# Optimization experiments

Measured on AMD Instinct MI355X. Metric: run time of the kernel, lower is better.

## Reference

```python
import jax, jax.numpy as jnp
import numpy as np

BS, H, W = 2, 24, 24
WIDTH = 20
M1 = M2 = 12
N = H * W
NPAIR = N * (N - 1) // 2
COLL_COEF = 0.9  # training=True path (eval path zeroes the collision term entirely)
_IU, _JU = np.triu_indices(N, k=1)  # static pair indices


def _gelu(x):
    return jax.nn.gelu(x, approximate=False)  # torch F.gelu default = exact erf


def _spectral(x, wr, wi):
    # x: (bs, c, h, w); wr/wi: (2, c, c, M1, M2) -> weights1, weights2
    bs, c, h, w = x.shape
    xft = jnp.fft.rfft2(x)  # (bs, c, h, w//2+1) complex64
    w1 = wr[0] + 1j * wi[0]
    w2 = wr[1] + 1j * wi[1]
    top = jnp.einsum('bixy,ioxy->boxy', xft[:, :, :M1, :M2], w1)
    bot = jnp.einsum('bixy,ioxy->boxy', xft[:, :, -M1:, :M2], w2)
    out = jnp.zeros((bs, c, h, w // 2 + 1), dtype=xft.dtype)
    out = out.at[:, :, :M1, :M2].set(top).at[:, :, -M1:, :M2].set(bot)
    return jnp.fft.irfft2(out, s=(h, w))


def _pair_norm(d):
    # d: (bs, c, n, n) -> (bs, n, n); eps keeps grad finite on the zero diagonal
    return jnp.sqrt(jnp.sum(d * d, axis=1) + 1e-12)


def _kinet_dsmc(p, a, vec):
    # p plays the role of x-positions; v = a*dt (dt=1) exactly as in the torch code
    bs, c, h, w = p.shape
    n = h * w
    x = p.reshape(bs, c, n)
    v = a.reshape(bs, c, n)  # v = a * dt
    x_r = _pair_norm(x[:, :, :, None] - x[:, :, None, :])       # (bs, n, n)
    v_r = _pair_norm(v[:, :, :, None] - v[:, :, None, :])       # (bs, n, n)
    v_cm = (v[:, :, :, None] + v[:, :, None, :]) * 0.5          # (bs, c, n, n)
    u_x = jnp.exp(-x_r)
    v_r_max = jnp.max(v_r, axis=(1, 2), keepdims=True)          # (bs, 1, 1)
    mask = v_r / v_r_max * u_x
    cmask = (mask > 1.0 - COLL_COEF).astype(p.dtype)            # (bs, n, n)
    # antisymmetric projection: R[:, :, i, j] = vec_pair for i<j, -vec_pair for i>j, 0 diag
    R = jnp.zeros((bs, c, n, n), p.dtype)
    R = R.at[:, :, _IU, _JU].set(vec).at[:, :, _JU, _IU].set(-vec)
    v_r_leaving = v_r[:, None] * R                               # (bs, c, n, n)
    delta_v = v_cm + v_r_leaving - v[:, :, :, None]
    v_new = v + jnp.sum(delta_v * cmask[:, None], axis=2)
    x_new = x + v_new  # dt = 1
    return x_new.reshape(bs, c, h, w), v_new.reshape(bs, c, h, w)


def _rv_step(rv, ori, s):
    rv = rv * ori + ori + s
    return rv / jnp.linalg.norm(rv, axis=1, keepdims=True)


def _forward(x, v, fc0_w, fc0_b, sc_wr, sc_wi, w_k, w_b, fc1_w, fc1_b, fc2_w, fc2_b, rv_init, rv_s):
    bs, h, w, _ = x.shape
    gx = jnp.broadcast_to(jnp.linspace(0.0, 1.0, h, dtype=x.dtype)[None, :, None, None], (bs, h, w, 1))
    gy = jnp.broadcast_to(jnp.linspace(0.0, 1.0, w, dtype=x.dtype)[None, None, :, None], (bs, h, w, 1))
    x = jnp.concatenate([x, gx, gy], axis=-1)          # (bs, h, w, 12)
    x = x @ fc0_w + fc0_b                              # lift to width
    x = jnp.transpose(x, (0, 3, 1, 2))                 # (bs, width, h, w)
    ori = rv_init / jnp.linalg.norm(rv_init, axis=1, keepdims=True)
    rv = rv_init
    for k in range(4):
        a = _spectral(x, sc_wr[k], sc_wi[k])
        p = jnp.einsum('bchw,oc->bohw', x, w_k[k]) + w_b[k][None, :, None, None]
        rv = _rv_step(rv, ori, rv_s[k])
        x, v = _kinet_dsmc(p, a, rv)
        if k < 3:
            x = _gelu(x)
            v = _gelu(v)
    x = jnp.transpose(x, (0, 2, 3, 1))                 # (bs, h, w, width)
    x = _gelu(x @ fc1_w + fc1_b)
    x = x @ fc2_w + fc2_b
    return x


def setup_inputs() -> dict:
    key = jax.random.key(0)
    ks = jax.random.split(key, 12)
    f = jnp.float32
    scale = 1.0 / (WIDTH * WIDTH)
    xs = -4.0 - 3.0 * jax.random.uniform(ks[9], (4,), f)                 # in [-7, -4]
    signs = jax.random.randint(ks[10], (4,), 0, 2).astype(f) * 2.0 - 1.0
    return {
        'x': jax.random.normal(ks[0], (BS, H, W, 10), f),
        'v': jax.random.normal(ks[1], (BS, WIDTH, H, W), f),
        'fc0_w': jax.random.normal(ks[2], (12, WIDTH), f) * 0.1,
        'fc0_b': jnp.zeros((WIDTH,), f),
        'sc_wr': jax.random.uniform(ks[3], (4, 2, WIDTH, WIDTH, M1, M2), f) * scale,
        'sc_wi': jax.random.uniform(ks[4], (4, 2, WIDTH, WIDTH, M1, M2), f) * scale,
        'w_k': jax.random.normal(ks[5], (4, WIDTH, WIDTH), f) * 0.1,
        'w_b': jnp.zeros((4, WIDTH), f),
        'fc1_w': jax.random.normal(ks[6], (WIDTH, 128), f) * 0.1,
        'fc1_b': jnp.zeros((128,), f),
        'fc2_w': jax.random.normal(ks[7], (128, 1), f) * 0.1,
        'fc2_b': jnp.zeros((1,), f),
        'rv_init': jax.random.normal(ks[8], (BS, WIDTH, NPAIR), f),
        'rv_s': signs * jnp.exp(xs),
    }


def reference(x, v, fc0_w, fc0_b, sc_wr, sc_wi, w_k, w_b, fc1_w, fc1_b, fc2_w, fc2_b, rv_init, rv_s):
    return _forward(x, v, fc0_w, fc0_b, sc_wr, sc_wi, w_k, w_b, fc1_w, fc1_b, fc2_w, fc2_b, rv_init, rv_s)
```

## Files before the change

kernel.cpp:

```cpp
#include <hip/hip_runtime.h>


#define N_     576
#define NPAIR_ 165600
#define C_     20
#define NB_TR  1294

__device__ __forceinline__ float gelu_f(float x){
    return 0.5f * x * (1.0f + erff(x * 0.70710678118654752440f));
}

__global__ void k_pre(const float* __restrict__ rvi, float* __restrict__ rvt,
                      const float* __restrict__ xin, const float* __restrict__ w,
                      const float* __restrict__ b, float* __restrict__ xo){
    int bid = blockIdx.x;
    if (bid < NB_TR){
        int t = bid*256 + threadIdx.x;
        if (t >= 2*NPAIR_) return;
        int bb = t / NPAIR_; int pr = t % NPAIR_;
        size_t ibase = (size_t)bb*C_*NPAIR_ + pr;
        float v[C_];
        #pragma unroll
        for (int c=0;c<C_;c++) v[c] = rvi[ibase + (size_t)c*NPAIR_];
        float4* dst = (float4*)(rvt + (size_t)t*C_);
        #pragma unroll
        for (int q=0;q<5;q++) dst[q] = make_float4(v[4*q],v[4*q+1],v[4*q+2],v[4*q+3]);
    } else {
        int t = (bid-NB_TR)*256 + threadIdx.x;
        if (t >= 2*N_) return;
        int hw = t % N_;
        int h = hw / 24, wc = hw % 24;
        float in[12];
        const float* xp = xin + (size_t)t*10;
        #pragma unroll
        for (int q=0;q<10;q++) in[q] = xp[q];
        in[10] = (float)h  * (1.0f/23.0f);
        in[11] = (float)wc * (1.0f/23.0f);
        #pragma unroll
        for (int c=0;c<C_;c++){
            float acc = b[c];
            #pragma unroll
            for (int q=0;q<12;q++) acc += in[q]*w[q*C_+c];
            xo[(size_t)(t/N_)*C_*N_ + (size_t)c*N_ + hw] = acc;
        }
    }
}

__global__ void k_specp(const float* __restrict__ x, float* __restrict__ Xr, float* __restrict__ Xi,
                        const float* __restrict__ wk, const float* __restrict__ wb,
                        float* __restrict__ p_t){
    if (blockIdx.x < 40){
        __shared__ float xt[576], Tr[288], Ti[288], cst[24], snt[24];
        int bc = blockIdx.x;
        int tid = threadIdx.x;
        if (tid < 24){
            float s, c;
            sincosf((float)tid * 0.26179938779914943654f, &s, &c);
            cst[tid]=c; snt[tid]=s;
        }
        for (int q=tid;q<576;q+=288) xt[q] = x[(size_t)bc*576+q];
        __syncthreads();
        {
            int h = tid/12, ky = tid%12;
            float ar=0.f, ai=0.f;
            for (int w=0;w<24;w++){
                int m = (ky*w) % 24;
                float v = xt[h*24+w];
                ar += v*cst[m];
                ai -= v*snt[m];
            }
            Tr[tid]=ar; Ti[tid]=ai;
        }
        __syncthreads();
        {
            int kx = tid/12, ky = tid%12;
            float ar=0.f, ai=0.f;
            for (int h=0;h<24;h++){
                int m = (kx*h)%24;
                float tr=Tr[h*12+ky], ti=Ti[h*12+ky];
                float cc=cst[m], ss=snt[m];
                ar += tr*cc + ti*ss;
                ai += ti*cc - tr*ss;
            }
            Xr[(size_t)bc*288 + tid] = ar;
            Xi[(size_t)bc*288 + tid] = ai;
        }
    } else {
        __shared__ float swk[400], swb[C_];
        int tid = threadIdx.x;
        for (int q=tid;q<400;q+=288) swk[q]=wk[q];
        if (tid < C_) swb[tid]=wb[tid];
        __syncthreads();
        int t = (blockIdx.x-40)*288 + tid;
        if (t >= 2*N_) return;
        int bb = t / N_, hw = t % N_;
        float xi[C_];
        #pragma unroll
        for (int c=0;c<C_;c++) xi[c] = x[(size_t)(bb*C_+c)*N_+hw];
        float accv[C_];
        #pragma unroll
        for (int o=0;o<C_;o++){
            float acc = swb[o];
            #pragma unroll
            for (int c=0;c<C_;c++) acc += xi[c]*swk[o*C_+c];
            accv[o]=acc;
        }
        float4* dst = (float4*)(p_t + (size_t)t*C_);
        #pragma unroll
        for (int q=0;q<5;q++) dst[q] = make_float4(accv[4*q],accv[4*q+1],accv[4*q+2],accv[4*q+3]);
    }
}

__global__ void k_fft_inv(const float* __restrict__ Xr, const float* __restrict__ Xi,
                          const float* __restrict__ wr, const float* __restrict__ wi,
                          float* __restrict__ a_t){
    __shared__ float Fr[288], Fi[288], Yr[288], Yi[288], cst[24], snt[24];
    int bo = blockIdx.x; int bb = bo/20, o = bo%20;
    int tid = threadIdx.x;
    if (tid < 24){
        float s, c;
        sincosf((float)tid * 0.26179938779914943654f, &s, &c);
        cst[tid]=c; snt[tid]=s;
    }
    if (tid < 288){
        int ky = tid%12, kx = tid/12;
        int half = (kx>=12) ? 1 : 0; int mx = kx - half*12;
        float ar=0.f, ai=0.f;
        for (int i=0;i<20;i++){
            float xr = Xr[(size_t)(bb*20+i)*288 + tid];
            float xi = Xi[(size_t)(bb*20+i)*288 + tid];
            size_t widx = ((((size_t)half*20+i)*20+o)*12+mx)*12+ky;
            float wrv = wr[widx], wiv = wi[widx];
            ar += xr*wrv - xi*wiv;
            ai += xr*wiv + xi*wrv;
        }
        Fr[tid]=ar; Fi[tid]=ai;
    }
    __syncthreads();
    if (tid < 288){
        int h = tid/12;
        float ar=0.f, ai=0.f;
        for (int kx=0;kx<24;kx++){
            int m=(kx*h)%24;
            float fr=Fr[kx*12 + (tid%12)], fi=Fi[kx*12 + (tid%12)];
            ar += fr*cst[m] - fi*snt[m];
            ai += fr*snt[m] + fi*cst[m];
        }
        Yr[tid]=ar*(1.0f/24.0f); Yi[tid]=ai*(1.0f/24.0f);
    }
    __syncthreads();
    {
        int h = tid/24, w = tid%24;
        float acc = Yr[h*12+0];
        #pragma unroll
        for (int ky=1;ky<12;ky++){
            int m=(ky*w)%24;
            acc += 2.0f*(Yr[h*12+ky]*cst[m] - Yi[h*12+ky]*snt[m]);
        }
        a_t[((size_t)bb*N_ + tid)*C_ + o] = acc*(1.0f/24.0f);
    }
}

__global__ void k_pairmax(const float* __restrict__ a_t, float* __restrict__ vmax){
    __shared__ float ai[C_], wred[9];
    int bb = blockIdx.x/N_, i = blockIdx.x%N_;
    int j = threadIdx.x;
    if (j < C_) ai[j]=a_t[((size_t)bb*N_+i)*C_+j];
    __syncthreads();
    const float4* aj4 = (const float4*)(a_t + ((size_t)bb*N_+j)*C_);
    float ssv=0.f;
    #pragma unroll
    for (int q=0;q<5;q++){
        float4 av = aj4[q];
        float dv;
        dv = ai[4*q+0]-av.x; ssv += dv*dv;
        dv = ai[4*q+1]-av.y; ssv += dv*dv;
        dv = ai[4*q+2]-av.z; ssv += dv*dv;
        dv = ai[4*q+3]-av.w; ssv += dv*dv;
    }
    float m = sqrtf(ssv+1e-12f);
    #pragma unroll
    for (int off=32; off; off>>=1) m = fmaxf(m, __shfl_down(m, off, 64));
    if ((j&63)==0) wred[j>>6] = m;
    __syncthreads();
    if (j==0){
        float mm = wred[0];
        #pragma unroll
        for (int q=1;q<9;q++) mm = fmaxf(mm, wred[q]);
        atomicMax((unsigned int*)&vmax[bb], __float_as_uint(mm));
    }
}

__global__ void __launch_bounds__(256, 1)
k_vnew(const float* __restrict__ p_t, const float* __restrict__ a_t,
       const float* __restrict__ rvt, const float* __restrict__ vmax,
       const float* __restrict__ rs, int klayer,
       float* __restrict__ xout, int do_gelu){
    __shared__ float pi[C_], ai[C_];
    __shared__ short hlist[N_];
    __shared__ int cnts[4];
    __shared__ float wacc[4][C_];
    int bb = blockIdx.x/N_, i = blockIdx.x%N_;
    int tid = threadIdx.x;
    int wid = tid>>6, lane = tid&63;
    if (tid < C_){ pi[tid]=p_t[((size_t)bb*N_+i)*C_+tid]; ai[tid]=a_t[((size_t)bb*N_+i)*C_+tid]; }
    __syncthreads();
    float vm = vmax[bb];
    const float thr = 0.1f;
    const float4* pbase = (const float4*)(p_t + (size_t)bb*N_*C_);
    const float4* abase = (const float4*)(a_t + (size_t)bb*N_*C_);

    int jb = wid*144;
    unsigned long long m0, m1, m2;
    {
        auto test = [&](int j)->bool{
            const float4* pj = pbase + j*5;
            const float4* aj = abase + j*5;
            float ssx=0.f, ssv=0.f;
            #pragma unroll
            for (int q=0;q<5;q++){
                float4 pv = pj[q], av = aj[q];
                float dx, dv;
                dx = pi[4*q+0]-pv.x; dv = ai[4*q+0]-av.x; ssx += dx*dx; ssv += dv*dv;
                dx = pi[4*q+1]-pv.y; dv = ai[4*q+1]-av.y; ssx += dx*dx; ssv += dv*dv;
                dx = pi[4*q+2]-pv.z; dv = ai[4*q+2]-av.z; ssx += dx*dx; ssv += dv*dv;
                dx = pi[4*q+3]-pv.w; dv = ai[4*q+3]-av.w; ssx += dx*dx; ssv += dv*dv;
            }
            float vrv = sqrtf(ssv+1e-12f);
            float uxv = expf(-sqrtf(ssx+1e-12f));
            return ((vrv/vm)*uxv > thr) && (j != i);
        };
        int j = jb + lane;
        m0 = __ballot(test(j));
        m1 = __ballot(test(j+64));
        bool h2 = (lane<16) ? test(jb+128+lane) : false;
        m2 = __ballot(h2);
    }
    if (lane == 0) cnts[wid] = (int)(__popcll(m0)+__popcll(m1)+__popcll(m2));
    __syncthreads();
    int off = 0;
    #pragma unroll
    for (int w=0;w<4;w++) if (w < wid) off += cnts[w];
    int nhit = cnts[0]+cnts[1]+cnts[2]+cnts[3];
    {
        unsigned long long below = (1ULL<<lane)-1ULL;
        int base = off;
        if (m0 & (1ULL<<lane)) hlist[base + __popcll(m0 & below)] = (short)(jb + lane);
        base += (int)__popcll(m0);
        if (m1 & (1ULL<<lane)) hlist[base + __popcll(m1 & below)] = (short)(jb + 64 + lane);
        base += (int)__popcll(m1);
        if (m2 & (1ULL<<lane)) hlist[base + __popcll(m2 & below)] = (short)(jb + 128 + lane);
    }
    __syncthreads();

    float s_arr[4] = { rs[0], rs[1], rs[2], rs[3] };
    float macc[C_];
    #pragma unroll
    for (int c=0;c<C_;c++) macc[c]=0.f;

    for (int t=tid; t<nhit; t+=256){
        int j = hlist[t];
        float av[C_];
        {
            const float4* aj = abase + j*5;
            #pragma unroll
            for (int q=0;q<5;q++){
                float4 aa = aj[q];
                av[4*q+0]=aa.x; av[4*q+1]=aa.y; av[4*q+2]=aa.z; av[4*q+3]=aa.w;
            }
        }
        float ssv=0.f;
        #pragma unroll
        for (int c=0;c<C_;c++){ float dv = ai[c]-av[c]; ssv += dv*dv; }
        float vrij = sqrtf(ssv+1e-12f);
        float sgn = (j<i) ? 1.0f : -1.0f;
        int lo = (j<i)?j:i, hi = (j<i)?i:j;
        int pidx = lo*(2*N_-lo-1)/2 + (hi-lo-1);
        float vrs = sgn*vrij;
        float st[C_];
        {
            const float4* rp = (const float4*)(rvt + ((size_t)bb*NPAIR_ + pidx)*C_);
            #pragma unroll
            for (int q=0;q<5;q++){
                float4 rr = rp[q];
                st[4*q+0]=rr.x; st[4*q+1]=rr.y; st[4*q+2]=rr.z; st[4*q+3]=rr.w;
            }
        }
        float ssq = 0.f;
        #pragma unroll
        for (int c=0;c<C_;c++) ssq += st[c]*st[c];
        float ini = 1.0f/sqrtf(ssq);
        float orc[C_];
        #pragma unroll
        for (int c=0;c<C_;c++) orc[c] = st[c]*ini;
        for (int l=0; l<=klayer; l++){
            float s = s_arr[l];
            float nq = 0.f;
            #pragma unroll
            for (int c=0;c<C_;c++){
                float nv = st[c]*orc[c] + orc[c] + s;
                st[c] = nv; nq += nv*nv;
            }
            float inn = 1.0f/sqrtf(nq);
            #pragma unroll
            for (int c=0;c<C_;c++) st[c] *= inn;
        }
        #pragma unroll
        for (int c=0;c<C_;c++) macc[c] += vrs*st[c] - 0.5f*av[c];
    }
    #pragma unroll
    for (int off2=32; off2; off2>>=1){
        #pragma unroll
        for (int c=0;c<C_;c++) macc[c] += __shfl_xor(macc[c], off2, 64);
    }
    if (lane == 0){
        #pragma unroll
        for (int c=0;c<C_;c++) wacc[wid][c] = macc[c];
    }
    __syncthreads();
    if (tid < C_){
        int c = tid;
        float msum = wacc[0][c]+wacc[1][c]+wacc[2][c]+wacc[3][c];
        float cnt = (float)nhit;
        float vi = ai[c];
        float vnew = vi + 0.5f*cnt*vi + msum;
        float xn = pi[c] + vnew;
        if (do_gelu) xn = gelu_f(xn);
        xout[(size_t)(bb*C_+c)*N_+i] = xn;
    }
}

__global__ void k_head(const float* __restrict__ x, const float* __restrict__ w1,
                       const float* __restrict__ b1, const float* __restrict__ w2,
                       const float* __restrict__ b2, float* __restrict__ out){
    __shared__ float xi[C_];
    __shared__ float part[2];
    int pos = blockIdx.x; int bb = pos/N_, hw = pos%N_;
    int t = threadIdx.x;
    if (t < C_) xi[t] = x[(size_t)(bb*C_+t)*N_+hw];
    __syncthreads();
    float h = b1[t];
    #pragma unroll
    for (int c=0;c<C_;c++) h += xi[c]*w1[c*128+t];
    float g = gelu_f(h) * w2[t];
    #pragma unroll
    for (int off=32; off; off>>=1) g += __shfl_down(g, off, 64);
    if ((t&63)==0) part[t>>6] = g;
    __syncthreads();
    if (t==0) out[pos] = part[0] + part[1] + b2[0];
}

extern "C" void kernel_launch(void* const* d_in, const int* in_sizes, int n_in,
                              void* d_out, int out_size, void* d_ws, size_t ws_size,
                              hipStream_t stream) {
    const float* in_x   = (const float*)d_in[0];
    const float* fc0_w  = (const float*)d_in[2];
    const float* fc0_b  = (const float*)d_in[3];
    const float* sc_wr  = (const float*)d_in[4];
    const float* sc_wi  = (const float*)d_in[5];
    const float* w_k    = (const float*)d_in[6];
    const float* w_b    = (const float*)d_in[7];
    const float* fc1_w  = (const float*)d_in[8];
    const float* fc1_b  = (const float*)d_in[9];
    const float* fc2_w  = (const float*)d_in[10];
    const float* fc2_b  = (const float*)d_in[11];
    const float* rv_init= (const float*)d_in[12];
    const float* rv_s   = (const float*)d_in[13];
    float* out = (float*)d_out;
    float* ws  = (float*)d_ws;

    float* x_cur = ws;
    float* p_t   = ws + 23040;
    float* a_t   = ws + 46080;
    float* Xr    = ws + 69120;
    float* Xi    = ws + 80640;
    float* rvt   = ws + 92160;
    float* vmax  = ws + 6716160;

    hipMemsetAsync(vmax, 0, 8*sizeof(float), stream);

    k_pre<<<NB_TR+5, 256, 0, stream>>>(rv_init, rvt, in_x, fc0_w, fc0_b, x_cur);

    for (int k=0;k<4;k++){
        const size_t woff = (size_t)k*2*20*20*144;
        k_specp<<<44, 288, 0, stream>>>(x_cur, Xr, Xi, w_k + k*400, w_b + k*20, p_t);
        k_fft_inv<<<40, 576, 0, stream>>>(Xr, Xi, sc_wr+woff, sc_wi+woff, a_t);
        k_pairmax<<<2*N_, N_, 0, stream>>>(a_t, vmax + 2*k);
        k_vnew<<<2*N_, 256, 0, stream>>>(p_t, a_t, rvt, vmax + 2*k, rv_s, k, x_cur, (k<3) ? 1 : 0);
    }

    k_head<<<2*N_, 128, 0, stream>>>(x_cur, fc1_w, fc1_b, fc2_w, fc2_b, out);
}
```

Measured before the change: 228.8 us.

## Fuse whole forward pass into one cooperative persistent kernel with grid syncs

Replaces the 18 separate launches (pre-transpose, per-layer spectral/FFT, pair max, collision update, head) with a single cooperative kernel of 256 blocks that uses grid.sync between stages. The head MLP is folded into the last layer's collision step. The aim is to remove launch overhead and inter-kernel gaps in a latency-bound pipeline. In exchange, the small FFT stages now run on only 40 of 256 blocks with 256 threads instead of 576, grid-wide barriers carry their own cost, and the old multi-kernel path is kept as a fallback if the cooperative launch fails.

```diff
diff --git a/kernel.cpp b/kernel.cpp
--- a/kernel.cpp
+++ b/kernel.cpp
@@ -1,13 +1,372 @@
 #include <hip/hip_runtime.h>
+#include <hip/hip_cooperative_groups.h>
+
+namespace cg = cooperative_groups;
 
 
 #define N_     576
 #define NPAIR_ 165600
 #define C_     20
+#define NB     256
+#define NT     256
 #define NB_TR  1294
 
 __device__ __forceinline__ float gelu_f(float x){
     return 0.5f * x * (1.0f + erff(x * 0.70710678118654752440f));
+}
+
+__global__ void __launch_bounds__(NT, 2)
+k_mega(const float* __restrict__ rvi,  const float* __restrict__ xin,
+       const float* __restrict__ fc0w, const float* __restrict__ fc0b,
+       const float* __restrict__ scwr, const float* __restrict__ scwi,
+       const float* __restrict__ wk,   const float* __restrict__ wb,
+       const float* __restrict__ fc1w, const float* __restrict__ fc1b,
+       const float* __restrict__ fc2w, const float* __restrict__ fc2b,
+       const float* __restrict__ rs,
+       float* __restrict__ rvt, float* __restrict__ x_cur,
+       float* __restrict__ p_t, float* __restrict__ a_t,
+       float* __restrict__ Xr,  float* __restrict__ Xi,
+       float* __restrict__ vmax, float* __restrict__ out)
+{
+    cg::grid_group grid = cg::this_grid();
+    __shared__ float sA[576], sB[288], sC[288], sD[288], sE[288];
+    __shared__ float cst[24], snt[24];
+    __shared__ short hlist[N_];
+    __shared__ int   cnts[4];
+    __shared__ float wacc[4][C_];
+    __shared__ float prow[C_], arow[C_];
+    __shared__ float wred[4];
+    __shared__ float psum[2];
+
+    const int tid = threadIdx.x;
+    const int bid = blockIdx.x;
+    const int wid = tid>>6, lane = tid&63;
+    const float sl0 = rs[0], sl1 = rs[1], sl2 = rs[2], sl3 = rs[3];
+
+    if (tid < 24){
+        float s, c;
+        sincosf((float)tid * 0.26179938779914943654f, &s, &c);
+        cst[tid]=c; snt[tid]=s;
+    }
+    __syncthreads();
+
+    for (int t = bid*NT + tid; t < 2*NPAIR_; t += NB*NT){
+        int bb = t / NPAIR_, pr = t % NPAIR_;
+        size_t ibase = (size_t)bb*C_*NPAIR_ + pr;
+        float v[C_];
+        #pragma unroll
+        for (int c=0;c<C_;c++) v[c] = rvi[ibase + (size_t)c*NPAIR_];
+        float4* dst = (float4*)(rvt + (size_t)t*C_);
+        #pragma unroll
+        for (int q=0;q<5;q++) dst[q] = make_float4(v[4*q],v[4*q+1],v[4*q+2],v[4*q+3]);
+    }
+    if (bid >= NB-5){
+        int t = (bid-(NB-5))*NT + tid;
+        if (t < 2*N_){
+            int hw = t % N_;
+            int h = hw/24, wc2 = hw%24;
+            float in[12];
+            const float* xp = xin + (size_t)t*10;
+            #pragma unroll
+            for (int q=0;q<10;q++) in[q]=xp[q];
+            in[10] = (float)h   * (1.0f/23.0f);
+            in[11] = (float)wc2 * (1.0f/23.0f);
+            #pragma unroll
+            for (int c=0;c<C_;c++){
+                float acc = fc0b[c];
+                #pragma unroll
+                for (int q=0;q<12;q++) acc += in[q]*fc0w[q*C_+c];
+                x_cur[(size_t)(t/N_)*C_*N_ + (size_t)c*N_ + hw] = acc;
+            }
+        }
+    }
+    grid.sync();
+
+    for (int kk=0; kk<4; ++kk){
+        const float* wkk = wk + kk*400;
+        const float* wbk = wb + kk*20;
+        const float* wrk = scwr + (size_t)kk*115200;
+        const float* wik = scwi + (size_t)kk*115200;
+
+        if (bid < 40){
+            for (int q=tid;q<576;q+=NT) sA[q] = x_cur[(size_t)bid*576+q];
+            __syncthreads();
+            for (int idx=tid; idx<288; idx+=NT){
+                int h=idx/12, ky=idx%12;
+                float ar=0.f, ai=0.f;
+                for (int w=0;w<24;w++){
+                    int m=(ky*w)%24;
+                    float v=sA[h*24+w];
+                    ar += v*cst[m];
+                    ai -= v*snt[m];
+                }
+                sB[idx]=ar; sC[idx]=ai;
+            }
+            __syncthreads();
+            for (int idx=tid; idx<288; idx+=NT){
+                int kx=idx/12, ky=idx%12;
+                float ar=0.f, ai=0.f;
+                for (int h=0;h<24;h++){
+                    int m=(kx*h)%24;
+                    float tr=sB[h*12+ky], ti=sC[h*12+ky];
+                    float cc=cst[m], ss=snt[m];
+                    ar += tr*cc + ti*ss;
+                    ai += ti*cc - tr*ss;
+                }
+                Xr[(size_t)bid*288+idx]=ar;
+                Xi[(size_t)bid*288+idx]=ai;
+            }
+        }
+        if (bid >= NB-5){
+            int t=(bid-(NB-5))*NT+tid;
+            if (t < 2*N_){
+                int bb=t/N_, hw=t%N_;
+                float xi20[C_];
+                #pragma unroll
+                for (int c=0;c<C_;c++) xi20[c]=x_cur[(size_t)(bb*C_+c)*N_+hw];
+                float accv[C_];
+                #pragma unroll
+                for (int o=0;o<C_;o++){
+                    float acc=wbk[o];
+                    #pragma unroll
+                    for (int c=0;c<C_;c++) acc += xi20[c]*wkk[o*C_+c];
+                    accv[o]=acc;
+                }
+                float4* dst=(float4*)(p_t+(size_t)t*C_);
+                #pragma unroll
+                for (int q=0;q<5;q++) dst[q]=make_float4(accv[4*q],accv[4*q+1],accv[4*q+2],accv[4*q+3]);
+            }
+        }
+        grid.sync();
+
+        if (bid < 40){
+            int bb=bid/20, o=bid%20;
+            for (int idx=tid; idx<288; idx+=NT){
+                int ky=idx%12, kx=idx/12;
+                int half=(kx>=12)?1:0; int mx=kx-half*12;
+                float ar=0.f, ai=0.f;
+                for (int i2=0;i2<20;i2++){
+                    float xr =Xr[(size_t)(bb*20+i2)*288+idx];
+                    float xiv=Xi[(size_t)(bb*20+i2)*288+idx];
+                    size_t widx=((((size_t)half*20+i2)*20+o)*12+mx)*12+ky;
+                    float wrv=wrk[widx], wiv=wik[widx];
+                    ar += xr*wrv - xiv*wiv;
+                    ai += xr*wiv + xiv*wrv;
+                }
+                sB[idx]=ar; sC[idx]=ai;
+            }
+            __syncthreads();
+            for (int idx=tid; idx<288; idx+=NT){
+                int h=idx/12, ky=idx%12;
+                float ar=0.f, ai=0.f;
+                for (int kx=0;kx<24;kx++){
+                    int m=(kx*h)%24;
+                    float fr=sB[kx*12+ky], fi=sC[kx*12+ky];
+                    ar += fr*cst[m] - fi*snt[m];
+                    ai += fr*snt[m] + fi*cst[m];
+                }
+                sD[idx]=ar*(1.0f/24.0f); sE[idx]=ai*(1.0f/24.0f);
+            }
+            __syncthreads();
+            for (int idx=tid; idx<576; idx+=NT){
+                int h=idx/24, w=idx%24;
+                float acc=sD[h*12];
+                #pragma unroll
+                for (int ky=1;ky<12;ky++){
+                    int m=(ky*w)%24;
+                    acc += 2.0f*(sD[h*12+ky]*cst[m] - sE[h*12+ky]*snt[m]);
+                }
+                a_t[((size_t)bb*N_+idx)*C_+o] = acc*(1.0f/24.0f);
+            }
+        }
+        grid.sync();
+
+        for (int row=bid; row<2*N_; row+=NB){
+            int bb=row/N_, i=row%N_;
+            if (tid<C_) arow[tid]=a_t[((size_t)bb*N_+i)*C_+tid];
+            __syncthreads();
+            const float4* abase=(const float4*)(a_t+(size_t)bb*N_*C_);
+            float mloc=0.f;
+            for (int j=tid;j<N_;j+=NT){
+                const float4* aj=abase+j*5;
+                float ssv=0.f;
+                #pragma unroll
+                for (int q=0;q<5;q++){
+                    float4 av=aj[q];
+                    float dv;
+                    dv=arow[4*q+0]-av.x; ssv+=dv*dv;
+                    dv=arow[4*q+1]-av.y; ssv+=dv*dv;
+                    dv=arow[4*q+2]-av.z; ssv+=dv*dv;
+                    dv=arow[4*q+3]-av.w; ssv+=dv*dv;
+                }
+                mloc=fmaxf(mloc, sqrtf(ssv+1e-12f));
+            }
+            #pragma unroll
+            for (int off=32; off; off>>=1) mloc=fmaxf(mloc,__shfl_down(mloc,off,64));
+            if (lane==0) wred[wid]=mloc;
+            __syncthreads();
+            if (tid==0){
+                float mm=fmaxf(fmaxf(wred[0],wred[1]),fmaxf(wred[2],wred[3]));
+                atomicMax((unsigned int*)&vmax[2*kk+bb], __float_as_uint(mm));
+            }
+            __syncthreads();
+        }
+        grid.sync();
+
+        for (int row=bid; row<2*N_; row+=NB){
+            int bb=row/N_, i=row%N_;
+            if (tid<C_){
+                prow[tid]=p_t[((size_t)bb*N_+i)*C_+tid];
+                arow[tid]=a_t[((size_t)bb*N_+i)*C_+tid];
+            }
+            __syncthreads();
+            float vm = vmax[2*kk+bb];
+            const float thr = 0.1f;
+            const float4* pbase=(const float4*)(p_t+(size_t)bb*N_*C_);
+            const float4* abase=(const float4*)(a_t+(size_t)bb*N_*C_);
+            int jb=wid*144;
+            unsigned long long m0,m1,m2;
+            {
+                auto test=[&](int j)->bool{
+                    const float4* pj=pbase+j*5;
+                    const float4* aj=abase+j*5;
+                    float ssx=0.f, ssv=0.f;
+                    #pragma unroll
+                    for (int q=0;q<5;q++){
+                        float4 pv=pj[q], av=aj[q];
+                        float dx,dv;
+                        dx=prow[4*q+0]-pv.x; dv=arow[4*q+0]-av.x; ssx+=dx*dx; ssv+=dv*dv;
+                        dx=prow[4*q+1]-pv.y; dv=arow[4*q+1]-av.y; ssx+=dx*dx; ssv+=dv*dv;
+                        dx=prow[4*q+2]-pv.z; dv=arow[4*q+2]-av.z; ssx+=dx*dx; ssv+=dv*dv;
+                        dx=prow[4*q+3]-pv.w; dv=arow[4*q+3]-av.w; ssx+=dx*dx; ssv+=dv*dv;
+                    }
+                    float vrv=sqrtf(ssv+1e-12f);
+                    float uxv=expf(-sqrtf(ssx+1e-12f));
+                    return ((vrv/vm)*uxv > thr) && (j != i);
+                };
+                int j=jb+lane;
+                m0=__ballot(test(j));
+                m1=__ballot(test(j+64));
+                bool h2=(lane<16)?test(jb+128+lane):false;
+                m2=__ballot(h2);
+            }
+            if (lane==0) cnts[wid]=(int)(__popcll(m0)+__popcll(m1)+__popcll(m2));
+            __syncthreads();
+            int off0=0;
+            #pragma unroll
+            for (int w2=0;w2<4;w2++) if (w2<wid) off0+=cnts[w2];
+            int nhit=cnts[0]+cnts[1]+cnts[2]+cnts[3];
+            {
+                unsigned long long below=(1ULL<<lane)-1ULL;
+                int base=off0;
+                if (m0&(1ULL<<lane)) hlist[base+__popcll(m0&below)]=(short)(jb+lane);
+                base+=(int)__popcll(m0);
+                if (m1&(1ULL<<lane)) hlist[base+__popcll(m1&below)]=(short)(jb+64+lane);
+                base+=(int)__popcll(m1);
+                if (m2&(1ULL<<lane)) hlist[base+__popcll(m2&below)]=(short)(jb+128+lane);
+            }
+            __syncthreads();
+
+            float macc[C_];
+            #pragma unroll
+            for (int c=0;c<C_;c++) macc[c]=0.f;
+            for (int t=tid; t<nhit; t+=NT){
+                int j=hlist[t];
+                float ssv=0.f;
+                {
+                    const float4* aj=abase+j*5;
+                    #pragma unroll
+                    for (int q=0;q<5;q++){
+                        float4 aa=aj[q];
+                        float dv;
+                        dv=arow[4*q+0]-aa.x; ssv+=dv*dv; macc[4*q+0]-=0.5f*aa.x;
+                        dv=arow[4*q+1]-aa.y; ssv+=dv*dv; macc[4*q+1]-=0.5f*aa.y;
+                        dv=arow[4*q+2]-aa.z; ssv+=dv*dv; macc[4*q+2]-=0.5f*aa.z;
+                        dv=arow[4*q+3]-aa.w; ssv+=dv*dv; macc[4*q+3]-=0.5f*aa.w;
+                    }
+                }
+                float vrij=sqrtf(ssv+1e-12f);
+                float sgn=(j<i)?1.0f:-1.0f;
+                int lo=(j<i)?j:i, hi=(j<i)?i:j;
+                int pidx=lo*(2*N_-lo-1)/2+(hi-lo-1);
+                float vrs=sgn*vrij;
+                float st[C_];
+                {
+                    const float4* rp=(const float4*)(rvt+((size_t)bb*NPAIR_+pidx)*C_);
+                    #pragma unroll
+                    for (int q=0;q<5;q++){
+                        float4 rr=rp[q];
+                        st[4*q+0]=rr.x; st[4*q+1]=rr.y; st[4*q+2]=rr.z; st[4*q+3]=rr.w;
+                    }
+                }
+                float ssq=0.f;
+                #pragma unroll
+                for (int c=0;c<C_;c++) ssq+=st[c]*st[c];
+                float ini=1.0f/sqrtf(ssq);
+                float orc[C_];
+                #pragma unroll
+                for (int c=0;c<C_;c++) orc[c]=st[c]*ini;
+                for (int l=0;l<=kk;l++){
+                    float s=(l==0)?sl0:((l==1)?sl1:((l==2)?sl2:sl3));
+                    float nq=0.f;
+                    #pragma unroll
+                    for (int c=0;c<C_;c++){
+                        float nv=st[c]*orc[c]+orc[c]+s;
+                        st[c]=nv; nq+=nv*nv;
+                    }
+                    float inn=1.0f/sqrtf(nq);
+                    #pragma unroll
+                    for (int c=0;c<C_;c++) st[c]*=inn;
+                }
+                #pragma unroll
+                for (int c=0;c<C_;c++) macc[c]+=vrs*st[c];
+            }
+            #pragma unroll
+            for (int off2=32; off2; off2>>=1){
+                #pragma unroll
+                for (int c=0;c<C_;c++) macc[c]+=__shfl_xor(macc[c],off2,64);
+            }
+            if (lane==0){
+                #pragma unroll
+                for (int c=0;c<C_;c++) wacc[wid][c]=macc[c];
+            }
+            __syncthreads();
+            if (kk<3){
+                if (tid<C_){
+                    int c=tid;
+                    float msum=wacc[0][c]+wacc[1][c]+wacc[2][c]+wacc[3][c];
+                    float vi=arow[c];
+                    float vnew=vi+0.5f*(float)nhit*vi+msum;
+                    float xn=prow[c]+vnew;
+                    x_cur[(size_t)(bb*C_+c)*N_+i]=gelu_f(xn);
+                }
+                __syncthreads();
+            } else {
+                if (tid<C_){
+                    int c=tid;
+                    float msum=wacc[0][c]+wacc[1][c]+wacc[2][c]+wacc[3][c];
+                    float vi=arow[c];
+                    float vnew=vi+0.5f*(float)nhit*vi+msum;
+                    sA[c]=prow[c]+vnew;
+                }
+                __syncthreads();
+                float g=0.f;
+                if (tid<128){
+                    float h=fc1b[tid];
+                    #pragma unroll
+                    for (int c=0;c<C_;c++) h+=sA[c]*fc1w[c*128+tid];
+                    g=gelu_f(h)*fc2w[tid];
+                    #pragma unroll
+                    for (int off2=32; off2; off2>>=1) g+=__shfl_down(g,off2,64);
+                    if (lane==0) psum[wid]=g;
+                }
+                __syncthreads();
+                if (tid==0) out[row]=psum[0]+psum[1]+fc2b[0];
+                __syncthreads();
+            }
+        }
+        if (kk<3) grid.sync();
+    }
 }
 
 __global__ void k_pre(const float* __restrict__ rvi, float* __restrict__ rvt,
@@ -369,25 +728,35 @@
     float* out = (float*)d_out;
     float* ws  = (float*)d_ws;
 
-    float* x_cur = ws;
-    float* p_t   = ws + 23040;
-    float* a_t   = ws + 46080;
-    float* Xr    = ws + 69120;
-    float* Xi    = ws + 80640;
-    float* rvt   = ws + 92160;
+    float* rvt   = ws;
+    float* x_cur = ws + 6624000;
+    float* p_t   = ws + 6647040;
+    float* a_t   = ws + 6670080;
+    float* Xr    = ws + 6693120;
+    float* Xi    = ws + 6704640;
     float* vmax  = ws + 6716160;
 
     hipMemsetAsync(vmax, 0, 8*sizeof(float), stream);
 
-    k_pre<<<NB_TR+5, 256, 0, stream>>>(rv_init, rvt, in_x, fc0_w, fc0_b, x_cur);
-
-    for (int k=0;k<4;k++){
-        const size_t woff = (size_t)k*2*20*20*144;
-        k_specp<<<44, 288, 0, stream>>>(x_cur, Xr, Xi, w_k + k*400, w_b + k*20, p_t);
-        k_fft_inv<<<40, 576, 0, stream>>>(Xr, Xi, sc_wr+woff, sc_wi+woff, a_t);
-        k_pairmax<<<2*N_, N_, 0, stream>>>(a_t, vmax + 2*k);
-        k_vnew<<<2*N_, 256, 0, stream>>>(p_t, a_t, rvt, vmax + 2*k, rv_s, k, x_cur, (k<3) ? 1 : 0);
-    }
-
-    k_head<<<2*N_, 128, 0, stream>>>(x_cur, fc1_w, fc1_b, fc2_w, fc2_b, out);
-}
+    void* args[] = {
+        (void*)&rv_init, (void*)&in_x, (void*)&fc0_w, (void*)&fc0_b,
+        (void*)&sc_wr, (void*)&sc_wi, (void*)&w_k, (void*)&w_b,
+        (void*)&fc1_w, (void*)&fc1_b, (void*)&fc2_w, (void*)&fc2_b,
+        (void*)&rv_s,
+        (void*)&rvt, (void*)&x_cur, (void*)&p_t, (void*)&a_t,
+        (void*)&Xr, (void*)&Xi, (void*)&vmax, (void*)&out
+    };
+    hipError_t err = hipLaunchCooperativeKernel((void*)k_mega, dim3(NB), dim3(NT), args, 0, stream);
+
+    if (err != hipSuccess){
+        k_pre<<<NB_TR+5, 256, 0, stream>>>(rv_init, rvt, in_x, fc0_w, fc0_b, x_cur);
+        for (int k=0;k<4;k++){
+            const size_t woff = (size_t)k*2*20*20*144;
+            k_specp<<<44, 288, 0, stream>>>(x_cur, Xr, Xi, w_k + k*400, w_b + k*20, p_t);
+            k_fft_inv<<<40, 576, 0, stream>>>(Xr, Xi, sc_wr+woff, sc_wi+woff, a_t);
+            k_pairmax<<<2*N_, N_, 0, stream>>>(a_t, vmax + 2*k);
+            k_vnew<<<2*N_, 256, 0, stream>>>(p_t, a_t, rvt, vmax + 2*k, rv_s, k, x_cur, (k<3) ? 1 : 0);
+        }
+        k_head<<<2*N_, 128, 0, stream>>>(x_cur, fc1_w, fc1_b, fc2_w, fc2_b, out);
+    }
+}
```

New measurement: 748.8 us. 227% more time.

## Fuse forward FFT, spectral mixing and inverse FFT; fold head into last vnew

Applied to the files above, without the earlier changes.

Merges the forward DFT kernel and the inverse-FFT/weight-mix kernel into one k_spec launch per layer. Each of the 40 blocks owns one (batch, output channel) pair and recomputes the forward DFT of all 20 input channels, two at a time, accumulating the complex weight products in shared memory. The separate head kernel is folded into the final k_vnew launch. This removes three launches per layer and the Xr/Xi round trip through global memory, at the cost of redundant forward transforms (20x more) and a serial 10-iteration loop per block.

```diff
diff --git a/kernel.cpp b/kernel.cpp
--- a/kernel.cpp
+++ b/kernel.cpp
@@ -46,52 +46,92 @@
     }
 }
 
-__global__ void k_specp(const float* __restrict__ x, float* __restrict__ Xr, float* __restrict__ Xi,
-                        const float* __restrict__ wk, const float* __restrict__ wb,
-                        float* __restrict__ p_t){
+__global__ void __launch_bounds__(576, 1)
+k_spec(const float* __restrict__ x, const float* __restrict__ wr, const float* __restrict__ wi,
+       const float* __restrict__ wk, const float* __restrict__ wb,
+       float* __restrict__ p_t, float* __restrict__ a_t){
     if (blockIdx.x < 40){
-        __shared__ float xt[576], Tr[288], Ti[288], cst[24], snt[24];
-        int bc = blockIdx.x;
+        __shared__ float cst[24], snt[24];
+        __shared__ float xch[1152];
+        __shared__ float Tr[576], Ti[576];
+        __shared__ float Fr[576], Fi[576];
+        int bb = blockIdx.x/20, o = blockIdx.x%20;
         int tid = threadIdx.x;
+        int half2 = tid/288, t2 = tid%288;
         if (tid < 24){
             float s, c;
             sincosf((float)tid * 0.26179938779914943654f, &s, &c);
             cst[tid]=c; snt[tid]=s;
         }
-        for (int q=tid;q<576;q+=288) xt[q] = x[(size_t)bc*576+q];
+        Fr[tid]=0.f; Fi[tid]=0.f;
+        __syncthreads();
+        for (int it=0; it<10; ++it){
+            for (int q=tid; q<1152; q+=576)
+                xch[q] = x[((size_t)bb*C_ + 2*it + q/576)*N_ + (q%576)];
+            __syncthreads();
+            {
+                int h=t2/12, ky=t2%12;
+                const float* xc = xch + half2*576;
+                float ar=0.f, ai=0.f;
+                for (int w2=0;w2<24;w2++){
+                    int m=(ky*w2)%24;
+                    float v=xc[h*24+w2];
+                    ar += v*cst[m];
+                    ai -= v*snt[m];
+                }
+                Tr[half2*288+t2]=ar; Ti[half2*288+t2]=ai;
+            }
+            __syncthreads();
+            {
+                int kx=t2/12, ky=t2%12;
+                float ar=0.f, ai=0.f;
+                for (int h=0;h<24;h++){
+                    int m=(kx*h)%24;
+                    float tr=Tr[half2*288+h*12+ky], ti=Ti[half2*288+h*12+ky];
+                    float cc=cst[m], ss=snt[m];
+                    ar += tr*cc + ti*ss;
+                    ai += ti*cc - tr*ss;
+                }
+                int i2 = 2*it + half2;
+                int hf=(kx>=12)?1:0; int mx=kx-hf*12;
+                size_t widx=((((size_t)hf*20+i2)*20+o)*12+mx)*12+ky;
+                float wrv=wr[widx], wiv=wi[widx];
+                Fr[half2*288+t2] += ar*wrv - ai*wiv;
+                Fi[half2*288+t2] += ar*wiv + ai*wrv;
+            }
+            __syncthreads();
+        }
+        if (tid<288){ Fr[tid]+=Fr[288+tid]; Fi[tid]+=Fi[288+tid]; }
+        __syncthreads();
+        if (tid<288){
+            int h=tid/12, ky=tid%12;
+            float ar=0.f, ai=0.f;
+            for (int kx=0;kx<24;kx++){
+                int m=(kx*h)%24;
+                float fr=Fr[kx*12+ky], fi=Fi[kx*12+ky];
+                ar += fr*cst[m] - fi*snt[m];
+                ai += fr*snt[m] + fi*cst[m];
+            }
+            xch[tid]=ar*(1.0f/24.0f); xch[288+tid]=ai*(1.0f/24.0f);
+        }
         __syncthreads();
         {
-            int h = tid/12, ky = tid%12;
-            float ar=0.f, ai=0.f;
-            for (int w=0;w<24;w++){
-                int m = (ky*w) % 24;
-                float v = xt[h*24+w];
-                ar += v*cst[m];
-                ai -= v*snt[m];
-            }
-            Tr[tid]=ar; Ti[tid]=ai;
-        }
-        __syncthreads();
-        {
-            int kx = tid/12, ky = tid%12;
-            float ar=0.f, ai=0.f;
-            for (int h=0;h<24;h++){
-                int m = (kx*h)%24;
-                float tr=Tr[h*12+ky], ti=Ti[h*12+ky];
-                float cc=cst[m], ss=snt[m];
-                ar += tr*cc + ti*ss;
-                ai += ti*cc - tr*ss;
-            }
-            Xr[(size_t)bc*288 + tid] = ar;
-            Xi[(size_t)bc*288 + tid] = ai;
+            int h=tid/24, w2=tid%24;
+            float acc=xch[h*12];
+            #pragma unroll
+            for (int ky=1;ky<12;ky++){
+                int m=(ky*w2)%24;
+                acc += 2.0f*(xch[h*12+ky]*cst[m] - xch[288+h*12+ky]*snt[m]);
+            }
+            a_t[((size_t)bb*N_+tid)*C_+o] = acc*(1.0f/24.0f);
         }
     } else {
         __shared__ float swk[400], swb[C_];
         int tid = threadIdx.x;
-        for (int q=tid;q<400;q+=288) swk[q]=wk[q];
+        for (int q=tid;q<400;q+=576) swk[q]=wk[q];
         if (tid < C_) swb[tid]=wb[tid];
         __syncthreads();
-        int t = (blockIdx.x-40)*288 + tid;
+        int t = (blockIdx.x-40)*576 + tid;
         if (t >= 2*N_) return;
         int bb = t / N_, hw = t % N_;
         float xi[C_];
@@ -108,56 +148,6 @@
         float4* dst = (float4*)(p_t + (size_t)t*C_);
         #pragma unroll
         for (int q=0;q<5;q++) dst[q] = make_float4(accv[4*q],accv[4*q+1],accv[4*q+2],accv[4*q+3]);
-    }
-}
-
-__global__ void k_fft_inv(const float* __restrict__ Xr, const float* __restrict__ Xi,
-                          const float* __restrict__ wr, const float* __restrict__ wi,
-                          float* __restrict__ a_t){
-    __shared__ float Fr[288], Fi[288], Yr[288], Yi[288], cst[24], snt[24];
-    int bo = blockIdx.x; int bb = bo/20, o = bo%20;
-    int tid = threadIdx.x;
-    if (tid < 24){
-        float s, c;
-        sincosf((float)tid * 0.26179938779914943654f, &s, &c);
-        cst[tid]=c; snt[tid]=s;
-    }
-    if (tid < 288){
-        int ky = tid%12, kx = tid/12;
-        int half = (kx>=12) ? 1 : 0; int mx = kx - half*12;
-        float ar=0.f, ai=0.f;
-        for (int i=0;i<20;i++){
-            float xr = Xr[(size_t)(bb*20+i)*288 + tid];
-            float xi = Xi[(size_t)(bb*20+i)*288 + tid];
-            size_t widx = ((((size_t)half*20+i)*20+o)*12+mx)*12+ky;
-            float wrv = wr[widx], wiv = wi[widx];
-            ar += xr*wrv - xi*wiv;
-            ai += xr*wiv + xi*wrv;
-        }
-        Fr[tid]=ar; Fi[tid]=ai;
-    }
-    __syncthreads();
-    if (tid < 288){
-        int h = tid/12;
-        float ar=0.f, ai=0.f;
-        for (int kx=0;kx<24;kx++){
-            int m=(kx*h)%24;
-            float fr=Fr[kx*12 + (tid%12)], fi=Fi[kx*12 + (tid%12)];
-            ar += fr*cst[m] - fi*snt[m];
-            ai += fr*snt[m] + fi*cst[m];
-        }
-        Yr[tid]=ar*(1.0f/24.0f); Yi[tid]=ai*(1.0f/24.0f);
-    }
-    __syncthreads();
-    {
-        int h = tid/24, w = tid%24;
-        float acc = Yr[h*12+0];
-        #pragma unroll
-        for (int ky=1;ky<12;ky++){
-            int m=(ky*w)%24;
-            acc += 2.0f*(Yr[h*12+ky]*cst[m] - Yi[h*12+ky]*snt[m]);
-        }
-        a_t[((size_t)bb*N_ + tid)*C_ + o] = acc*(1.0f/24.0f);
     }
 }
 
@@ -195,11 +185,16 @@
 k_vnew(const float* __restrict__ p_t, const float* __restrict__ a_t,
        const float* __restrict__ rvt, const float* __restrict__ vmax,
        const float* __restrict__ rs, int klayer,
-       float* __restrict__ xout, int do_gelu){
+       float* __restrict__ xout, int do_head,
+       const float* __restrict__ fc1w, const float* __restrict__ fc1b,
+       const float* __restrict__ fc2w, const float* __restrict__ fc2b,
+       float* __restrict__ out){
     __shared__ float pi[C_], ai[C_];
     __shared__ short hlist[N_];
     __shared__ int cnts[4];
     __shared__ float wacc[4][C_];
+    __shared__ float xrow[C_];
+    __shared__ float psum[2];
     int bb = blockIdx.x/N_, i = blockIdx.x%N_;
     int tid = threadIdx.x;
     int wid = tid>>6, lane = tid&63;
@@ -318,36 +313,36 @@
         for (int c=0;c<C_;c++) wacc[wid][c] = macc[c];
     }
     __syncthreads();
-    if (tid < C_){
-        int c = tid;
-        float msum = wacc[0][c]+wacc[1][c]+wacc[2][c]+wacc[3][c];
-        float cnt = (float)nhit;
-        float vi = ai[c];
-        float vnew = vi + 0.5f*cnt*vi + msum;
-        float xn = pi[c] + vnew;
-        if (do_gelu) xn = gelu_f(xn);
-        xout[(size_t)(bb*C_+c)*N_+i] = xn;
-    }
-}
-
-__global__ void k_head(const float* __restrict__ x, const float* __restrict__ w1,
-                       const float* __restrict__ b1, const float* __restrict__ w2,
-                       const float* __restrict__ b2, float* __restrict__ out){
-    __shared__ float xi[C_];
-    __shared__ float part[2];
-    int pos = blockIdx.x; int bb = pos/N_, hw = pos%N_;
-    int t = threadIdx.x;
-    if (t < C_) xi[t] = x[(size_t)(bb*C_+t)*N_+hw];
-    __syncthreads();
-    float h = b1[t];
-    #pragma unroll
-    for (int c=0;c<C_;c++) h += xi[c]*w1[c*128+t];
-    float g = gelu_f(h) * w2[t];
-    #pragma unroll
-    for (int off=32; off; off>>=1) g += __shfl_down(g, off, 64);
-    if ((t&63)==0) part[t>>6] = g;
-    __syncthreads();
-    if (t==0) out[pos] = part[0] + part[1] + b2[0];
+    if (!do_head){
+        if (tid < C_){
+            int c = tid;
+            float msum = wacc[0][c]+wacc[1][c]+wacc[2][c]+wacc[3][c];
+            float vi = ai[c];
+            float vnew = vi + 0.5f*(float)nhit*vi + msum;
+            float xn = pi[c] + vnew;
+            xout[(size_t)(bb*C_+c)*N_+i] = gelu_f(xn);
+        }
+    } else {
+        if (tid < C_){
+            int c = tid;
+            float msum = wacc[0][c]+wacc[1][c]+wacc[2][c]+wacc[3][c];
+            float vi = ai[c];
+            float vnew = vi + 0.5f*(float)nhit*vi + msum;
+            xrow[c] = pi[c] + vnew;
+        }
+        __syncthreads();
+        if (tid < 128){
+            float h = fc1b[tid];
+            #pragma unroll
+            for (int c=0;c<C_;c++) h += xrow[c]*fc1w[c*128+tid];
+            float g = gelu_f(h)*fc2w[tid];
+            #pragma unroll
+            for (int off2=32; off2; off2>>=1) g += __shfl_down(g, off2, 64);
+            if (lane==0) psum[wid] = g;
+        }
+        __syncthreads();
+        if (tid==0) out[bb*N_+i] = psum[0] + psum[1] + fc2b[0];
+    }
 }
 
 extern "C" void kernel_launch(void* const* d_in, const int* in_sizes, int n_in,
@@ -369,25 +364,23 @@
     float* out = (float*)d_out;
     float* ws  = (float*)d_ws;
 
-    float* x_cur = ws;
-    float* p_t   = ws + 23040;
-    float* a_t   = ws + 46080;
-    float* Xr    = ws + 69120;
-    float* Xi    = ws + 80640;
-    float* rvt   = ws + 92160;
-    float* vmax  = ws + 6716160;
+    float* rvt   = ws;
+    float* x_cur = ws + 6624000;
+    float* p_t   = ws + 6647040;
+    float* a_t   = ws + 6670080;
+    float* vmax  = ws + 6693120;
 
     hipMemsetAsync(vmax, 0, 8*sizeof(float), stream);
 
     k_pre<<<NB_TR+5, 256, 0, stream>>>(rv_init, rvt, in_x, fc0_w, fc0_b, x_cur);
 
     for (int k=0;k<4;k++){
-        const size_t woff = (size_t)k*2*20*20*144;
-        k_specp<<<44, 288, 0, stream>>>(x_cur, Xr, Xi, w_k + k*400, w_b + k*20, p_t);
-        k_fft_inv<<<40, 576, 0, stream>>>(Xr, Xi, sc_wr+woff, sc_wi+woff, a_t);
+        const size_t woff = (size_t)k*115200;
+        k_spec<<<42, 576, 0, stream>>>(x_cur, sc_wr+woff, sc_wi+woff,
+                                       w_k + k*400, w_b + k*20, p_t, a_t);
         k_pairmax<<<2*N_, N_, 0, stream>>>(a_t, vmax + 2*k);
-        k_vnew<<<2*N_, 256, 0, stream>>>(p_t, a_t, rvt, vmax + 2*k, rv_s, k, x_cur, (k<3) ? 1 : 0);
-    }
-
-    k_head<<<2*N_, 128, 0, stream>>>(x_cur, fc1_w, fc1_b, fc2_w, fc2_b, out);
-}
+        k_vnew<<<2*N_, 256, 0, stream>>>(p_t, a_t, rvt, vmax + 2*k, rv_s, k,
+                                         x_cur, (k==3) ? 1 : 0,
+                                         fc1_w, fc1_b, fc2_w, fc2_b, out);
+    }
+}
```

Result: slower. 297.9 us (+30.2%).

## Spread rv transpose across first-layer kernels and fuse head into last vnew

Applied to the files above, without the earlier changes.

The large rv_init transpose is no longer done in one up-front pre-kernel. Its blocks are appended as extra blocks to the under-filled first-layer launches (lift, forward spectral, inverse FFT, pairmax), so the memory-bound copy fills otherwise idle CUs alongside the small compute grids. Each kernel gets extra early-exit branches and pointer arguments, and the workspace layout is reordered. Separately, the final MLP head (fc1, gelu, fc2) is fused into the last k_vnew launch, which removes one launch and a round trip of x through global memory. The rvt data must be fully written before the first k_vnew reads it, which stream ordering guarantees.

```diff
diff --git a/kernel.cpp b/kernel.cpp
--- a/kernel.cpp
+++ b/kernel.cpp
@@ -4,51 +4,68 @@
 #define N_     576
 #define NPAIR_ 165600
 #define C_     20
-#define NB_TR  1294
+
+#define TR_LIFT_B 128
+#define TR_SPEC_B 384
+#define TR_INV_B  192
+#define TR_PMAX_B 144
+#define TR0 0
+#define TR1 (TR0 + TR_LIFT_B*256)
+#define TR2 (TR1 + TR_SPEC_B*288)
+#define TR3 (TR2 + TR_INV_B*576)
 
 __device__ __forceinline__ float gelu_f(float x){
     return 0.5f * x * (1.0f + erff(x * 0.70710678118654752440f));
 }
 
-__global__ void k_pre(const float* __restrict__ rvi, float* __restrict__ rvt,
-                      const float* __restrict__ xin, const float* __restrict__ w,
-                      const float* __restrict__ b, float* __restrict__ xo){
+__device__ __forceinline__ void tr_one(const float* __restrict__ rvi,
+                                       float* __restrict__ rvt, int t){
+    if (t >= 2*NPAIR_) return;
+    int bb = t / NPAIR_, pr = t % NPAIR_;
+    size_t ibase = (size_t)bb*C_*NPAIR_ + pr;
+    float v[C_];
+    #pragma unroll
+    for (int c=0;c<C_;c++) v[c] = rvi[ibase + (size_t)c*NPAIR_];
+    float4* dst = (float4*)(rvt + (size_t)t*C_);
+    #pragma unroll
+    for (int q=0;q<5;q++) dst[q] = make_float4(v[4*q],v[4*q+1],v[4*q+2],v[4*q+3]);
+}
+
+__global__ void k_lift(const float* __restrict__ xin, const float* __restrict__ w,
+                       const float* __restrict__ b, float* __restrict__ xo,
+                       const float* __restrict__ rvi, float* __restrict__ rvt){
     int bid = blockIdx.x;
-    if (bid < NB_TR){
-        int t = bid*256 + threadIdx.x;
-        if (t >= 2*NPAIR_) return;
-        int bb = t / NPAIR_; int pr = t % NPAIR_;
-        size_t ibase = (size_t)bb*C_*NPAIR_ + pr;
-        float v[C_];
-        #pragma unroll
-        for (int c=0;c<C_;c++) v[c] = rvi[ibase + (size_t)c*NPAIR_];
-        float4* dst = (float4*)(rvt + (size_t)t*C_);
-        #pragma unroll
-        for (int q=0;q<5;q++) dst[q] = make_float4(v[4*q],v[4*q+1],v[4*q+2],v[4*q+3]);
-    } else {
-        int t = (bid-NB_TR)*256 + threadIdx.x;
-        if (t >= 2*N_) return;
-        int hw = t % N_;
-        int h = hw / 24, wc = hw % 24;
-        float in[12];
-        const float* xp = xin + (size_t)t*10;
-        #pragma unroll
-        for (int q=0;q<10;q++) in[q] = xp[q];
-        in[10] = (float)h  * (1.0f/23.0f);
-        in[11] = (float)wc * (1.0f/23.0f);
-        #pragma unroll
-        for (int c=0;c<C_;c++){
-            float acc = b[c];
-            #pragma unroll
-            for (int q=0;q<12;q++) acc += in[q]*w[q*C_+c];
-            xo[(size_t)(t/N_)*C_*N_ + (size_t)c*N_ + hw] = acc;
-        }
+    if (bid >= 5){
+        tr_one(rvi, rvt, TR0 + (bid-5)*256 + (int)threadIdx.x);
+        return;
+    }
+    int t = bid*256 + threadIdx.x;
+    if (t >= 2*N_) return;
+    int hw = t % N_;
+    int h = hw / 24, wc = hw % 24;
+    float in[12];
+    const float* xp = xin + (size_t)t*10;
+    #pragma unroll
+    for (int q=0;q<10;q++) in[q] = xp[q];
+    in[10] = (float)h  * (1.0f/23.0f);
+    in[11] = (float)wc * (1.0f/23.0f);
+    #pragma unroll
+    for (int c=0;c<C_;c++){
+        float acc = b[c];
+        #pragma unroll
+        for (int q=0;q<12;q++) acc += in[q]*w[q*C_+c];
+        xo[(size_t)(t/N_)*C_*N_ + (size_t)c*N_ + hw] = acc;
     }
 }
 
 __global__ void k_specp(const float* __restrict__ x, float* __restrict__ Xr, float* __restrict__ Xi,
                         const float* __restrict__ wk, const float* __restrict__ wb,
-                        float* __restrict__ p_t){
+                        float* __restrict__ p_t,
+                        const float* __restrict__ rvi, float* __restrict__ rvt){
+    if (blockIdx.x >= 44){
+        tr_one(rvi, rvt, TR1 + (blockIdx.x-44)*288 + (int)threadIdx.x);
+        return;
+    }
     if (blockIdx.x < 40){
         __shared__ float xt[576], Tr[288], Ti[288], cst[24], snt[24];
         int bc = blockIdx.x;
@@ -113,7 +130,12 @@
 
 __global__ void k_fft_inv(const float* __restrict__ Xr, const float* __restrict__ Xi,
                           const float* __restrict__ wr, const float* __restrict__ wi,
-                          float* __restrict__ a_t){
+                          float* __restrict__ a_t,
+                          const float* __restrict__ rvi, float* __restrict__ rvt){
+    if (blockIdx.x >= 40){
+        tr_one(rvi, rvt, TR2 + (blockIdx.x-40)*576 + (int)threadIdx.x);
+        return;
+    }
     __shared__ float Fr[288], Fi[288], Yr[288], Yi[288], cst[24], snt[24];
     int bo = blockIdx.x; int bb = bo/20, o = bo%20;
     int tid = threadIdx.x;
@@ -161,7 +183,12 @@
     }
 }
 
-__global__ void k_pairmax(const float* __restrict__ a_t, float* __restrict__ vmax){
+__global__ void k_pairmax(const float* __restrict__ a_t, float* __restrict__ vmax,
+                          const float* __restrict__ rvi, float* __restrict__ rvt){
+    if (blockIdx.x >= 2*N_){
+        tr_one(rvi, rvt, TR3 + (blockIdx.x-2*N_)*576 + (int)threadIdx.x);
+        return;
+    }
     __shared__ float ai[C_], wred[9];
     int bb = blockIdx.x/N_, i = blockIdx.x%N_;
     int j = threadIdx.x;
@@ -195,11 +222,16 @@
 k_vnew(const float* __restrict__ p_t, const float* __restrict__ a_t,
        const float* __restrict__ rvt, const float* __restrict__ vmax,
        const float* __restrict__ rs, int klayer,
-       float* __restrict__ xout, int do_gelu){
+       float* __restrict__ xout, int do_head,
+       const float* __restrict__ fc1w, const float* __restrict__ fc1b,
+       const float* __restrict__ fc2w, const float* __restrict__ fc2b,
+       float* __restrict__ out){
     __shared__ float pi[C_], ai[C_];
     __shared__ short hlist[N_];
     __shared__ int cnts[4];
     __shared__ float wacc[4][C_];
+    __shared__ float xrow[C_];
+    __shared__ float psum[2];
     int bb = blockIdx.x/N_, i = blockIdx.x%N_;
     int tid = threadIdx.x;
     int wid = tid>>6, lane = tid&63;
@@ -318,36 +350,36 @@
         for (int c=0;c<C_;c++) wacc[wid][c] = macc[c];
     }
     __syncthreads();
-    if (tid < C_){
-        int c = tid;
-        float msum = wacc[0][c]+wacc[1][c]+wacc[2][c]+wacc[3][c];
-        float cnt = (float)nhit;
-        float vi = ai[c];
-        float vnew = vi + 0.5f*cnt*vi + msum;
-        float xn = pi[c] + vnew;
-        if (do_gelu) xn = gelu_f(xn);
-        xout[(size_t)(bb*C_+c)*N_+i] = xn;
-    }
-}
-
-__global__ void k_head(const float* __restrict__ x, const float* __restrict__ w1,
-                       const float* __restrict__ b1, const float* __restrict__ w2,
-                       const float* __restrict__ b2, float* __restrict__ out){
-    __shared__ float xi[C_];
-    __shared__ float part[2];
-    int pos = blockIdx.x; int bb = pos/N_, hw = pos%N_;
-    int t = threadIdx.x;
-    if (t < C_) xi[t] = x[(size_t)(bb*C_+t)*N_+hw];
-    __syncthreads();
-    float h = b1[t];
-    #pragma unroll
-    for (int c=0;c<C_;c++) h += xi[c]*w1[c*128+t];
-    float g = gelu_f(h) * w2[t];
-    #pragma unroll
-    for (int off=32; off; off>>=1) g += __shfl_down(g, off, 64);
-    if ((t&63)==0) part[t>>6] = g;
-    __syncthreads();
-    if (t==0) out[pos] = part[0] + part[1] + b2[0];
+    if (!do_head){
+        if (tid < C_){
+            int c = tid;
+            float msum = wacc[0][c]+wacc[1][c]+wacc[2][c]+wacc[3][c];
+            float vi = ai[c];
+            float vnew = vi + 0.5f*(float)nhit*vi + msum;
+            float xn = pi[c] + vnew;
+            xout[(size_t)(bb*C_+c)*N_+i] = gelu_f(xn);
+        }
+    } else {
+        if (tid < C_){
+            int c = tid;
+            float msum = wacc[0][c]+wacc[1][c]+wacc[2][c]+wacc[3][c];
+            float vi = ai[c];
+            float vnew = vi + 0.5f*(float)nhit*vi + msum;
+            xrow[c] = pi[c] + vnew;
+        }
+        __syncthreads();
+        if (tid < 128){
+            float h = fc1b[tid];
+            #pragma unroll
+            for (int c=0;c<C_;c++) h += xrow[c]*fc1w[c*128+tid];
+            float g = gelu_f(h)*fc2w[tid];
+            #pragma unroll
+            for (int off2=32; off2; off2>>=1) g += __shfl_down(g, off2, 64);
+            if (lane==0) psum[wid] = g;
+        }
+        __syncthreads();
+        if (tid==0) out[bb*N_+i] = psum[0] + psum[1] + fc2b[0];
+    }
 }
 
 extern "C" void kernel_launch(void* const* d_in, const int* in_sizes, int n_in,
@@ -369,25 +401,28 @@
     float* out = (float*)d_out;
     float* ws  = (float*)d_ws;
 
-    float* x_cur = ws;
-    float* p_t   = ws + 23040;
-    float* a_t   = ws + 46080;
-    float* Xr    = ws + 69120;
-    float* Xi    = ws + 80640;
-    float* rvt   = ws + 92160;
+    float* rvt   = ws;
+    float* x_cur = ws + 6624000;
+    float* p_t   = ws + 6647040;
+    float* a_t   = ws + 6670080;
+    float* Xr    = ws + 6693120;
+    float* Xi    = ws + 6704640;
     float* vmax  = ws + 6716160;
 
     hipMemsetAsync(vmax, 0, 8*sizeof(float), stream);
 
-    k_pre<<<NB_TR+5, 256, 0, stream>>>(rv_init, rvt, in_x, fc0_w, fc0_b, x_cur);
+    k_lift<<<5 + TR_LIFT_B, 256, 0, stream>>>(in_x, fc0_w, fc0_b, x_cur, rv_init, rvt);
 
     for (int k=0;k<4;k++){
-        const size_t woff = (size_t)k*2*20*20*144;
-        k_specp<<<44, 288, 0, stream>>>(x_cur, Xr, Xi, w_k + k*400, w_b + k*20, p_t);
-        k_fft_inv<<<40, 576, 0, stream>>>(Xr, Xi, sc_wr+woff, sc_wi+woff, a_t);
-        k_pairmax<<<2*N_, N_, 0, stream>>>(a_t, vmax + 2*k);
-        k_vnew<<<2*N_, 256, 0, stream>>>(p_t, a_t, rvt, vmax + 2*k, rv_s, k, x_cur, (k<3) ? 1 : 0);
-    }
-
-    k_head<<<2*N_, 128, 0, stream>>>(x_cur, fc1_w, fc1_b, fc2_w, fc2_b, out);
-}
+        const size_t woff = (size_t)k*115200;
+        int g_sp = (k==0) ? 44 + TR_SPEC_B : 44;
+        int g_iv = (k==0) ? 40 + TR_INV_B  : 40;
+        int g_pm = (k==0) ? 2*N_ + TR_PMAX_B : 2*N_;
+        k_specp<<<g_sp, 288, 0, stream>>>(x_cur, Xr, Xi, w_k + k*400, w_b + k*20, p_t, rv_init, rvt);
+        k_fft_inv<<<g_iv, 576, 0, stream>>>(Xr, Xi, sc_wr+woff, sc_wi+woff, a_t, rv_init, rvt);
+        k_pairmax<<<g_pm, N_, 0, stream>>>(a_t, vmax + 2*k, rv_init, rvt);
+        k_vnew<<<2*N_, 256, 0, stream>>>(p_t, a_t, rvt, vmax + 2*k, rv_s, k,
+                                         x_cur, (k==3) ? 1 : 0,
+                                         fc1_w, fc1_b, fc2_w, fc2_b, out);
+    }
+}
```

After: 217.7 us. 4.8% less time.
